# Kernel tuning notes

Measured on AMD Instinct MI355X. Metric: run time of the kernel, lower is better.

## Reference

```python
import jax, jax.numpy as jnp
import numpy as np
import math

NUM_HEADS = 16


def _alibi_slopes(n):
    # n is a power of 2 here (16)
    start = 2.0 ** (-2.0 ** (-(math.log2(n) - 3)))
    return jnp.asarray([start * (start ** i) for i in range(n)], dtype=jnp.float32)


def setup_inputs() -> dict:
    key = jax.random.key(0)
    ks = jax.random.split(key, 7)
    B, S, D = 2, 2048, 1024
    s = 0.02
    return {
        "query": jax.random.normal(ks[0], (B, S, D), jnp.float32),
        "key": jax.random.normal(ks[1], (B, S, D), jnp.float32),
        "value": jax.random.normal(ks[2], (B, S, D), jnp.float32),
        "Wq": jax.random.normal(ks[3], (D, D), jnp.float32) * s,
        "Wk": jax.random.normal(ks[4], (D, D), jnp.float32) * s,
        "Wv": jax.random.normal(ks[5], (D, D), jnp.float32) * s,
        "Wo": jax.random.normal(ks[6], (D, D), jnp.float32) * s,
    }


def reference(query, key, value, Wq, Wk, Wv, Wo):
    B, S, D = query.shape
    H = NUM_HEADS
    hd = D // H
    scale = math.sqrt(hd)

    # projections (bias-free linears), split into heads: [B, S, H, hd]
    Q = (query @ Wq).reshape(B, S, H, hd)
    K = (key @ Wk).reshape(B, -1, H, hd)
    V = (value @ Wv).reshape(B, -1, H, hd)

    # attention scores [B, H, S, S]
    scores = jnp.einsum("bqhd,bkhd->bhqk", Q, K) / scale

    # ALiBi bias: -slope_h * |i - j|, broadcast over batch
    pos = jnp.arange(S, dtype=jnp.float32)
    rel = jnp.abs(pos[None, :] - pos[:, None])  # [S, S]
    slopes = _alibi_slopes(H)
    scores = scores - slopes[None, :, None, None] * rel[None, None, :, :]

    attn = jax.nn.softmax(scores, axis=-1)
    out = jnp.einsum("bhqk,bkhd->bqhd", attn, V).reshape(B, S, D)
    return out @ Wo
```

## Files before the change

### kernel.cpp

```cpp
#include <hip/hip_runtime.h>
#include <cstdint>
#include <cstddef>


typedef unsigned short u16;
typedef __attribute__((ext_vector_type(8))) _Float16 half8;
typedef __attribute__((ext_vector_type(4))) float f32x4;

#define DEVI static __device__ __forceinline__
#define MFMA16(a, b, c) __builtin_amdgcn_mfma_f32_16x16x32_f16(a, b, c, 0, 0, 0)

DEVI u16 f2h_bits(float f) {
  _Float16 h = (_Float16)f;
  union { _Float16 h; u16 u; } v; v.h = h;
  return v.u;
}

DEVI void gl_lds16(const u16* g, u16* l) {
  __builtin_amdgcn_global_load_lds(
      (const __attribute__((address_space(1))) void*)g,
      (__attribute__((address_space(3))) void*)l, 16, 0, 0);
}

__global__ __launch_bounds__(256) void cast3_h(const float* __restrict__ in0,
                                               const float* __restrict__ in1,
                                               const float* __restrict__ in2,
                                               u16* __restrict__ o0,
                                               u16* __restrict__ o1,
                                               u16* __restrict__ o2, int n) {
  const float* in = blockIdx.z == 0 ? in0 : (blockIdx.z == 1 ? in1 : in2);
  u16* out = blockIdx.z == 0 ? o0 : (blockIdx.z == 1 ? o1 : o2);
  int i = (blockIdx.x * 256 + threadIdx.x) * 4;
  if (i + 3 < n) {
    const float4 v = *(const float4*)(in + i);
    ushort4 o;
    o.x = f2h_bits(v.x); o.y = f2h_bits(v.y); o.z = f2h_bits(v.z); o.w = f2h_bits(v.w);
    *(ushort4*)(out + i) = o;
  }
}

__global__ __launch_bounds__(256) void transpose4_h(
    const float* __restrict__ W0, const float* __restrict__ W1,
    const float* __restrict__ W2, const float* __restrict__ W3,
    u16* __restrict__ T0, u16* __restrict__ T1, u16* __restrict__ T2,
    u16* __restrict__ T3) {
  const float* W = blockIdx.z == 0 ? W0 : (blockIdx.z == 1 ? W1 : (blockIdx.z == 2 ? W2 : W3));
  u16* Wt = blockIdx.z == 0 ? T0 : (blockIdx.z == 1 ? T1 : (blockIdx.z == 2 ? T2 : T3));
  __shared__ float tile[32][33];
  const int bx = blockIdx.x * 32;
  const int by = blockIdx.y * 32;
  const int x = threadIdx.x & 31;
  const int y0 = threadIdx.x >> 5;
#pragma unroll
  for (int i = y0; i < 32; i += 8)
    tile[i][x] = W[(size_t)(by + i) * 1024 + bx + x];
  __syncthreads();
#pragma unroll
  for (int i = y0; i < 32; i += 8)
    Wt[(size_t)(bx + i) * 1024 + by + x] = f2h_bits(tile[x][i]);
}

DEVI void gemm_body(const u16* __restrict__ A, const u16* __restrict__ Bt,
                    void* __restrict__ Cout, int mode, u16* As, u16* Bs) {
  constexpr int K = 1024, N = 1024;
  const int t = threadIdx.x;
  const int lane = t & 63;
  const int quad = lane >> 4;
  const int l16 = lane & 15;
  const int wid = t >> 6;
  const int mBase = blockIdx.y * 128;
  const int nBase = blockIdx.x * 128;
  const int wM = (wid >> 1) * 64;
  const int wN = (wid & 1) * 64;
  const int aswz = (quad ^ ((l16 >> 1) & 3)) << 3;

  f32x4 acc[4][4];
#pragma unroll
  for (int i = 0; i < 4; ++i)
#pragma unroll
    for (int j = 0; j < 4; ++j) acc[i][j] = (f32x4){0.f, 0.f, 0.f, 0.f};

  for (int kt = 0; kt < K / 32; ++kt) {
    const int kB = kt * 32;
    __syncthreads();
#pragma unroll
    for (int i = 0; i < 2; ++i) {
      const int ci = i * 256 + t;
      const int row = ci >> 2;
      const int col = (((ci & 3) ^ ((ci >> 3) & 3)) << 3);
      gl_lds16(A + (size_t)(mBase + row) * K + kB + col, As + ci * 8);
      gl_lds16(Bt + (size_t)(nBase + row) * K + kB + col, Bs + ci * 8);
    }
    __syncthreads();

    half8 a[4], b[4];
#pragma unroll
    for (int mi = 0; mi < 4; ++mi)
      a[mi] = *(const half8*)(As + (wM + mi * 16 + l16) * 32 + aswz);
#pragma unroll
    for (int ni = 0; ni < 4; ++ni)
      b[ni] = *(const half8*)(Bs + (wN + ni * 16 + l16) * 32 + aswz);
#pragma unroll
    for (int mi = 0; mi < 4; ++mi)
#pragma unroll
      for (int ni = 0; ni < 4; ++ni)
        acc[mi][ni] = MFMA16(a[mi], b[ni], acc[mi][ni]);
  }

#pragma unroll
  for (int mi = 0; mi < 4; ++mi) {
#pragma unroll
    for (int ni = 0; ni < 4; ++ni) {
#pragma unroll
      for (int r = 0; r < 4; ++r) {
        const int m = mBase + wM + mi * 16 + quad * 4 + r;
        const int n = nBase + wN + ni * 16 + l16;
        const float v = acc[mi][ni][r];
        if (mode == 0) {
          ((float*)Cout)[(size_t)m * N + n] = v;
        } else if (mode == 1) {
          ((u16*)Cout)[(size_t)m * N + n] = f2h_bits(v);
        } else {
          ((u16*)Cout)[(((size_t)(m >> 11) * 1024 + n) << 11) | (size_t)(m & 2047)] = f2h_bits(v);
        }
      }
    }
  }
}

__global__ __launch_bounds__(256) void proj_qkv(
    const u16* __restrict__ qb, const u16* __restrict__ kb, const u16* __restrict__ vb,
    const u16* __restrict__ Wqt, const u16* __restrict__ Wkt, const u16* __restrict__ Wvt,
    u16* __restrict__ Qp, u16* __restrict__ Kp, u16* __restrict__ Vtp) {
  __shared__ u16 As[128 * 32];
  __shared__ u16 Bs[128 * 32];
  const int z = blockIdx.z;
  const u16* A = z == 0 ? qb : (z == 1 ? kb : vb);
  const u16* Bt = z == 0 ? Wqt : (z == 1 ? Wkt : Wvt);
  void* C = z == 0 ? (void*)Qp : (z == 1 ? (void*)Kp : (void*)Vtp);
  gemm_body(A, Bt, C, z == 2 ? 2 : 1, As, Bs);
}

__global__ __launch_bounds__(256) void gemm_out(const u16* __restrict__ Ao,
                                                const u16* __restrict__ Wot,
                                                float* __restrict__ out) {
  __shared__ u16 As[128 * 32];
  __shared__ u16 Bs[128 * 32];
  gemm_body(Ao, Wot, out, 0, As, Bs);
}

__global__ __launch_bounds__(128, 2) void flash_alibi(
    const u16* __restrict__ Qg, const u16* __restrict__ Kg,
    const u16* __restrict__ Vtg, u16* __restrict__ Og) {
  constexpr int S = 2048, Dm = 1024, HD = 64;
  __shared__ u16 Qs[64 * 64];
  __shared__ u16 Ks[64 * 64];
  __shared__ u16 Vs[64 * 64];
  __shared__ u16 Ps[64 * 64];
  const int t = threadIdx.x, lane = t & 63, wid = t >> 6;
  const int quad = lane >> 4, l16 = lane & 15;
  const int qt = blockIdx.x, h = blockIdx.y, b = blockIdx.z;
  const int qBase = qt * 64;
  const size_t qRow0 = (size_t)b * S + qBase;
  const float sl2 = __builtin_amdgcn_exp2f(-0.5f * (float)(h + 1)) * 1.44269504f;
  const float sc2 = 0.125f * 1.44269504f;
  const int Di = (int)(30.0f / sl2);
  const int ktLo = max(0, (qBase - Di) >> 6);
  const int ktHi = min(31, (qBase + 63 + Di) >> 6);
  const int cswz = ((l16 & 7) << 3);

#pragma unroll
  for (int i = 0; i < 4; ++i) {
    const int ci = i * 128 + t;
    const int row = ci >> 3, col = (((ci & 7) ^ (row & 7)) << 3);
    gl_lds16(Qg + (qRow0 + row) * Dm + h * HD + col, Qs + ci * 8);
  }

  float bi[2][4];
#pragma unroll
  for (int m = 0; m < 2; ++m)
#pragma unroll
    for (int r = 0; r < 4; ++r)
      bi[m][r] = sl2 * (float)(qBase + wid * 32 + m * 16 + quad * 4 + r);

  f32x4 acc_o[2][4];
#pragma unroll
  for (int m = 0; m < 2; ++m)
#pragma unroll
    for (int nd = 0; nd < 4; ++nd) acc_o[m][nd] = (f32x4){0.f, 0.f, 0.f, 0.f};
  float lrow[2][4] = {{0.f, 0.f, 0.f, 0.f}, {0.f, 0.f, 0.f, 0.f}};

  const int pRowBase = wid * 32;

  for (int kt = ktLo; kt <= ktHi; ++kt) {
    const int kB = kt * 64;
    __syncthreads();
#pragma unroll
    for (int i = 0; i < 4; ++i) {
      const int ci = i * 128 + t;
      const int row = ci >> 3, col = (((ci & 7) ^ (row & 7)) << 3);
      gl_lds16(Kg + ((size_t)b * S + kB + row) * Dm + h * HD + col, Ks + ci * 8);
      gl_lds16(Vtg + ((size_t)(b * 16 + h) * HD + row) * S + kB + col, Vs + ci * 8);
    }
    __syncthreads();

    f32x4 s[2][4];
#pragma unroll
    for (int m = 0; m < 2; ++m)
#pragma unroll
      for (int ni = 0; ni < 4; ++ni) s[m][ni] = (f32x4){0.f, 0.f, 0.f, 0.f};
#pragma unroll
    for (int ks = 0; ks < 2; ++ks) {
      const int ck = ((ks * 4 + quad) << 3) ^ cswz;
      const half8 a0 = *(const half8*)(Qs + (wid * 32 + l16) * HD + ck);
      const half8 a1 = *(const half8*)(Qs + (wid * 32 + 16 + l16) * HD + ck);
#pragma unroll
      for (int ni = 0; ni < 4; ++ni) {
        const half8 bk = *(const half8*)(Ks + (ni * 16 + l16) * HD + ck);
        s[0][ni] = MFMA16(a0, bk, s[0][ni]);
        s[1][ni] = MFMA16(a1, bk, s[1][ni]);
      }
    }

    float bj[4];
#pragma unroll
    for (int ni = 0; ni < 4; ++ni) bj[ni] = sl2 * (float)(kB + ni * 16 + l16);
#pragma unroll
    for (int m = 0; m < 2; ++m) {
#pragma unroll
      for (int r = 0; r < 4; ++r) {
        float rs = 0.f;
        const int prow = (pRowBase + m * 16 + quad * 4 + r) * 64;
#pragma unroll
        for (int ni = 0; ni < 4; ++ni) {
          const float d = fabsf(bi[m][r] - bj[ni]);
          const float p = __builtin_amdgcn_exp2f(s[m][ni][r] * sc2 - d);
          rs += p;
          Ps[prow + ((ni * 16 + l16) ^ (quad << 4))] = f2h_bits(p);
        }
        lrow[m][r] += rs;
      }
    }
    __asm__ volatile("s_waitcnt lgkmcnt(0)" ::: "memory");

#pragma unroll
    for (int ks = 0; ks < 2; ++ks) {
      const int pk = (ks * 32 + quad * 8) ^ ((l16 & 12) << 2);
      const int ck = ((ks * 4 + quad) << 3) ^ cswz;
      const half8 aP0 = *(const half8*)(Ps + (pRowBase + l16) * 64 + pk);
      const half8 aP1 = *(const half8*)(Ps + (pRowBase + 16 + l16) * 64 + pk);
#pragma unroll
      for (int nd = 0; nd < 4; ++nd) {
        const half8 bv = *(const half8*)(Vs + (nd * 16 + l16) * HD + ck);
        acc_o[0][nd] = MFMA16(aP0, bv, acc_o[0][nd]);
        acc_o[1][nd] = MFMA16(aP1, bv, acc_o[1][nd]);
      }
    }
  }

#pragma unroll
  for (int m = 0; m < 2; ++m) {
#pragma unroll
    for (int r = 0; r < 4; ++r) {
      float l = lrow[m][r];
      l += __shfl_xor(l, 1);
      l += __shfl_xor(l, 2);
      l += __shfl_xor(l, 4);
      l += __shfl_xor(l, 8);
      const float inv = 1.f / l;
      const int rloc = wid * 32 + m * 16 + quad * 4 + r;
#pragma unroll
      for (int nd = 0; nd < 4; ++nd)
        Og[(qRow0 + rloc) * Dm + h * HD + nd * 16 + l16] = f2h_bits(acc_o[m][nd][r] * inv);
    }
  }
}

extern "C" void kernel_launch(void* const* d_in, const int* in_sizes, int n_in,
                              void* d_out, int out_size, void* d_ws, size_t ws_size,
                              hipStream_t stream) {
  const float* q  = (const float*)d_in[0];
  const float* k  = (const float*)d_in[1];
  const float* v  = (const float*)d_in[2];
  const float* Wq = (const float*)d_in[3];
  const float* Wk = (const float*)d_in[4];
  const float* Wv = (const float*)d_in[5];
  const float* Wo = (const float*)d_in[6];
  char* ws = (char*)d_ws;
  const size_t MB = 1ull << 20;
  u16* qb  = (u16*)(ws + 0 * MB);
  u16* kb  = (u16*)(ws + 8 * MB);
  u16* vb  = (u16*)(ws + 16 * MB);
  u16* Wqt = (u16*)(ws + 24 * MB);
  u16* Wkt = (u16*)(ws + 26 * MB);
  u16* Wvt = (u16*)(ws + 28 * MB);
  u16* Wot = (u16*)(ws + 30 * MB);
  u16* Qp  = (u16*)(ws + 32 * MB);
  u16* Kp  = (u16*)(ws + 40 * MB);
  u16* Vtp = (u16*)(ws + 48 * MB);
  u16* Ao  = (u16*)(ws + 56 * MB);

  const int n = 2 * 2048 * 1024;
  cast3_h<<<dim3(n / 1024, 1, 3), 256, 0, stream>>>(q, k, v, qb, kb, vb, n);
  transpose4_h<<<dim3(32, 32, 4), 256, 0, stream>>>(Wq, Wk, Wv, Wo, Wqt, Wkt, Wvt, Wot);
  proj_qkv<<<dim3(8, 32, 3), 256, 0, stream>>>(qb, kb, vb, Wqt, Wkt, Wvt, Qp, Kp, Vtp);
  flash_alibi<<<dim3(32, 16, 2), 128, 0, stream>>>(Qp, Kp, Vtp, Ao);
  gemm_out<<<dim3(8, 32), 256, 0, stream>>>(Ao, Wot, (float*)d_out);
}
```

Measured before the change: 235.7 us.

## Split V transpose into separate kernel and reorder flash blocks by head workload

The V projection no longer writes a transposed layout with scattered 2-byte stores. It writes row-major output, and a new LDS-tiled kernel transposes it into the reused vb buffer with vectorized 16-byte stores. The flash attention grid is flattened and remapped so that heads with the widest ALiBi window (smallest slope, h=15) are launched first, which balances the tail. The cost is one extra kernel launch and an additional read and write pass over V.

New measurement: 240.3 us. No clear change (+2.0%).

```diff
diff --git a/kernel.cpp b/kernel.cpp
--- a/kernel.cpp
+++ b/kernel.cpp
@@ -5,6 +5,7 @@
 
 typedef unsigned short u16;
 typedef __attribute__((ext_vector_type(8))) _Float16 half8;
+typedef __attribute__((ext_vector_type(8))) unsigned short u16x8;
 typedef __attribute__((ext_vector_type(4))) float f32x4;
 
 #define DEVI static __device__ __forceinline__
@@ -60,6 +61,32 @@
     Wt[(size_t)(bx + i) * 1024 + by + x] = f2h_bits(tile[x][i]);
 }
 
+__global__ __launch_bounds__(256) void vtrans(const u16* __restrict__ Vp,
+                                              u16* __restrict__ Vt) {
+  __shared__ u16 tile[64][72];
+  const int t = threadIdx.x;
+  const int s0 = blockIdx.x * 64;
+  const int bh = blockIdx.y;
+  const int b = bh >> 4, h = bh & 15;
+#pragma unroll
+  for (int it = 0; it < 2; ++it) {
+    const int ci = it * 256 + t;
+    const int srow = ci >> 3, cc = (ci & 7) << 3;
+    const u16x8 v = *(const u16x8*)(Vp + (size_t)(b * 2048 + s0 + srow) * 1024 + h * 64 + cc);
+    *(u16x8*)(&tile[srow][cc]) = v;
+  }
+  __syncthreads();
+#pragma unroll
+  for (int it = 0; it < 2; ++it) {
+    const int ci = it * 256 + t;
+    const int drow = ci >> 3, cc = (ci & 7) << 3;
+    u16x8 o;
+#pragma unroll
+    for (int j = 0; j < 8; ++j) o[j] = tile[cc + j][drow];
+    *(u16x8*)(Vt + ((size_t)bh * 64 + drow) * 2048 + s0 + cc) = o;
+  }
+}
+
 DEVI void gemm_body(const u16* __restrict__ A, const u16* __restrict__ Bt,
                     void* __restrict__ Cout, int mode, u16* As, u16* Bs) {
   constexpr int K = 1024, N = 1024;
@@ -118,10 +145,8 @@
         const float v = acc[mi][ni][r];
         if (mode == 0) {
           ((float*)Cout)[(size_t)m * N + n] = v;
-        } else if (mode == 1) {
+        } else {
           ((u16*)Cout)[(size_t)m * N + n] = f2h_bits(v);
-        } else {
-          ((u16*)Cout)[(((size_t)(m >> 11) * 1024 + n) << 11) | (size_t)(m & 2047)] = f2h_bits(v);
         }
       }
     }
@@ -131,14 +156,14 @@
 __global__ __launch_bounds__(256) void proj_qkv(
     const u16* __restrict__ qb, const u16* __restrict__ kb, const u16* __restrict__ vb,
     const u16* __restrict__ Wqt, const u16* __restrict__ Wkt, const u16* __restrict__ Wvt,
-    u16* __restrict__ Qp, u16* __restrict__ Kp, u16* __restrict__ Vtp) {
+    u16* __restrict__ Qp, u16* __restrict__ Kp, u16* __restrict__ Vp) {
   __shared__ u16 As[128 * 32];
   __shared__ u16 Bs[128 * 32];
   const int z = blockIdx.z;
   const u16* A = z == 0 ? qb : (z == 1 ? kb : vb);
   const u16* Bt = z == 0 ? Wqt : (z == 1 ? Wkt : Wvt);
-  void* C = z == 0 ? (void*)Qp : (z == 1 ? (void*)Kp : (void*)Vtp);
-  gemm_body(A, Bt, C, z == 2 ? 2 : 1, As, Bs);
+  void* C = z == 0 ? (void*)Qp : (z == 1 ? (void*)Kp : (void*)Vp);
+  gemm_body(A, Bt, C, 1, As, Bs);
 }
 
 __global__ __launch_bounds__(256) void gemm_out(const u16* __restrict__ Ao,
@@ -159,7 +184,10 @@
   __shared__ u16 Ps[64 * 64];
   const int t = threadIdx.x, lane = t & 63, wid = t >> 6;
   const int quad = lane >> 4, l16 = lane & 15;
-  const int qt = blockIdx.x, h = blockIdx.y, b = blockIdx.z;
+  const int idx = blockIdx.x;
+  const int h = 15 - (idx >> 6);
+  const int qt = (idx >> 1) & 31;
+  const int b = idx & 1;
   const int qBase = qt * 64;
   const size_t qRow0 = (size_t)b * S + qBase;
   const float sl2 = __builtin_amdgcn_exp2f(-0.5f * (float)(h + 1)) * 1.44269504f;
@@ -297,13 +325,15 @@
   u16* Wot = (u16*)(ws + 30 * MB);
   u16* Qp  = (u16*)(ws + 32 * MB);
   u16* Kp  = (u16*)(ws + 40 * MB);
-  u16* Vtp = (u16*)(ws + 48 * MB);
+  u16* Vp  = (u16*)(ws + 48 * MB);
   u16* Ao  = (u16*)(ws + 56 * MB);
+  u16* Vt  = vb;
 
   const int n = 2 * 2048 * 1024;
   cast3_h<<<dim3(n / 1024, 1, 3), 256, 0, stream>>>(q, k, v, qb, kb, vb, n);
   transpose4_h<<<dim3(32, 32, 4), 256, 0, stream>>>(Wq, Wk, Wv, Wo, Wqt, Wkt, Wvt, Wot);
-  proj_qkv<<<dim3(8, 32, 3), 256, 0, stream>>>(qb, kb, vb, Wqt, Wkt, Wvt, Qp, Kp, Vtp);
-  flash_alibi<<<dim3(32, 16, 2), 128, 0, stream>>>(Qp, Kp, Vtp, Ao);
+  proj_qkv<<<dim3(8, 32, 3), 256, 0, stream>>>(qb, kb, vb, Wqt, Wkt, Wvt, Qp, Kp, Vp);
+  vtrans<<<dim3(32, 32), 256, 0, stream>>>(Vp, Vt);
+  flash_alibi<<<1024, 128, 0, stream>>>(Qp, Kp, Vt, Ao);
   gemm_out<<<dim3(8, 32), 256, 0, stream>>>(Ao, Wot, (float*)d_out);
 }
```
